# Kernel optimization log

Measured on AMD Instinct MI355X. Metric: run time of the kernel, lower is better.

The kernel has to match this reference:

```python
import jax, jax.numpy as jnp
import numpy as np

G = 8            # group_order
KS = 3           # kernel size
C1, O1 = 1, 16   # gconv1 channels
C2, O2 = 16, 32  # gconv2 channels
HW = 28
NUM_CLASSES = 10


def _bilinear_sample(img, px, py):
    # img: (O, I, K, K); px, py: (K, K) pixel coords; zero padding outside
    # (matches torch grid_sample bilinear, align_corners=False, padding_mode='zeros')
    K = img.shape[-1]
    x0 = jnp.floor(px); y0 = jnp.floor(py)
    wx = px - x0; wy = py - y0
    x0i = x0.astype(jnp.int32); y0i = y0.astype(jnp.int32)

    def gather(yi, xi):
        valid = (yi >= 0) & (yi < K) & (xi >= 0) & (xi < K)
        yc = jnp.clip(yi, 0, K - 1)
        xc = jnp.clip(xi, 0, K - 1)
        return img[:, :, yc, xc] * valid.astype(img.dtype)  # (O,I,K,K)

    return (gather(y0i, x0i) * (1 - wx) * (1 - wy)
            + gather(y0i, x0i + 1) * wx * (1 - wy)
            + gather(y0i + 1, x0i) * (1 - wx) * wy
            + gather(y0i + 1, x0i + 1) * wx * wy)


def _rotated_kernels(base, group_order):
    # Replicates F.affine_grid + F.grid_sample (align_corners=False) for each rotation k.
    K = base.shape[-1]
    coords = (2.0 * jnp.arange(K, dtype=base.dtype) + 1.0) / K - 1.0  # normalized centers
    xs, ys = jnp.meshgrid(coords, coords, indexing='xy')  # x along width, y along height

    def rot_k(k):
        theta = 2.0 * np.pi * k / group_order
        c, s = jnp.cos(theta), jnp.sin(theta)
        gx = c * xs - s * ys   # theta row [cos, -sin, 0]
        gy = s * xs + c * ys   # theta row [sin,  cos, 0]
        px = ((gx + 1.0) * K - 1.0) / 2.0  # unnormalize, align_corners=False
        py = ((gy + 1.0) * K - 1.0) / 2.0
        return _bilinear_sample(base, px, py)

    return jax.vmap(rot_k)(jnp.arange(group_order, dtype=base.dtype))  # (G,O,I,K,K)


def _conv2d(x, w, pad):
    return jax.lax.conv_general_dilated(
        x, w, window_strides=(1, 1), padding=[(pad, pad), (pad, pad)],
        dimension_numbers=('NCHW', 'OIHW', 'NCHW'))


def setup_inputs() -> dict:
    key = jax.random.key(0)
    k1, k2, k3, k4, k5 = jax.random.split(key, 5)
    x = jax.random.normal(k1, (512, C1, HW, HW), dtype=jnp.float32)
    base_weight = jax.random.normal(k2, (O1, C1, KS, KS), dtype=jnp.float32)
    w2 = jax.random.normal(k3, (O2, C2, G, KS, KS), dtype=jnp.float32) * 0.05
    fc_w = jax.random.normal(k4, (NUM_CLASSES, O2 * HW * HW), dtype=jnp.float32) * 0.01
    fc_b = jax.random.normal(k5, (NUM_CLASSES,), dtype=jnp.float32) * 0.01
    return {"x": x, "base_weight": base_weight, "w2": w2, "fc_w": fc_w, "fc_b": fc_b}


def reference(x, base_weight, w2, fc_w, fc_b):
    B = x.shape[0]
    # --- GroupConv2D: steerable rotated kernels, concat along out-channels (k-major) ---
    rk = _rotated_kernels(base_weight, G)           # (G, O1, C1, K, K)
    w1 = rk.reshape(G * O1, C1, KS, KS)
    h = _conv2d(x, w1, 1)                           # (B, G*O1, 28, 28)
    h = jax.nn.relu(h)                              # GroupReLU == plain ReLU

    # --- GroupToGroupConv: circulant structure fused into one conv ---
    # torch: out channel = g*O2 + o (cat dim=1), in channel = c*G + h_idx (view layout)
    g = jnp.arange(G)[:, None]
    hh = jnp.arange(G)[None, :]
    idx = (g - hh) % G                               # (G, G)
    Wc = w2[:, :, idx]                               # (O2, C2, G_g, G_h, K, K)
    Wbig = jnp.transpose(Wc, (2, 0, 1, 3, 4, 5)).reshape(G * O2, C2 * G, KS, KS)
    h2 = _conv2d(h, Wbig, 1)                         # (B, G*O2, 28, 28)
    h2 = jax.nn.relu(h2)

    # --- GroupPooling (mean over the *inner* factor of 8, as in the torch view) ---
    p = h2.reshape(B, (G * O2) // G, G, HW, HW).mean(axis=2)  # (B, 32, 28, 28)

    # --- fc ---
    flat = p.reshape(B, -1)
    return flat @ fc_w.T + fc_b
```

## Files before the change

### kernel.cpp

```cpp
#include <hip/hip_runtime.h>
#include <hip/hip_bf16.h>
#include <cstdint>

#define AS1 __attribute__((address_space(1)))
#define AS3 __attribute__((address_space(3)))

typedef __bf16 bf16x8 __attribute__((ext_vector_type(8)));
typedef float  f32x16 __attribute__((ext_vector_type(16)));

__device__ __forceinline__ void gld_lds16(const void* g, void* l) {
    __builtin_amdgcn_global_load_lds((const AS1 void*)g, (AS3 void*)l, 16, 0, 0);
}

__global__ void k_rot(const float* __restrict__ base, float* __restrict__ w1) {
    int m = threadIdx.x;
    int g = m >> 4, o = m & 15;
    float th = 6.28318530717958647692f * (float)g / 8.0f;
    float c = cosf(th), s = sinf(th);
    for (int i = 0; i < 3; ++i) {
        float ys = (2.0f * i + 1.0f) / 3.0f - 1.0f;
        for (int j = 0; j < 3; ++j) {
            float xs = (2.0f * j + 1.0f) / 3.0f - 1.0f;
            float gx = c * xs - s * ys;
            float gy = s * xs + c * ys;
            float px = ((gx + 1.0f) * 3.0f - 1.0f) * 0.5f;
            float py = ((gy + 1.0f) * 3.0f - 1.0f) * 0.5f;
            float x0 = floorf(px), y0 = floorf(py);
            float wx = px - x0, wy = py - y0;
            int x0i = (int)x0, y0i = (int)y0;
            auto gat = [&](int yi, int xi) -> float {
                bool v = (yi >= 0) && (yi < 3) && (xi >= 0) && (xi < 3);
                int yc = min(max(yi, 0), 2), xc = min(max(xi, 0), 2);
                return v ? base[o * 9 + yc * 3 + xc] : 0.0f;
            };
            w1[m * 9 + i * 3 + j] =
                  gat(y0i, x0i)         * (1.0f - wx) * (1.0f - wy)
                + gat(y0i, x0i + 1)     * wx          * (1.0f - wy)
                + gat(y0i + 1, x0i)     * (1.0f - wx) * wy
                + gat(y0i + 1, x0i + 1) * wx          * wy;
        }
    }
}

__global__ __launch_bounds__(256) void k_conv1(const float* __restrict__ x,
                                               const float* __restrict__ w1g,
                                               const float* __restrict__ w2,
                                               __hip_bfloat16* __restrict__ hl,
                                               __hip_bfloat16* __restrict__ A) {
    int tid = threadIdx.x;

    if (blockIdx.x < 1152) {
        int i = blockIdx.x * 256 + tid;
        int r = i / 1152, k = i - r * 1152;
        int g = r >> 5, o2 = r & 31;
        int kk = k >> 7, cch = k & 127;
        int ky = kk / 3, kx = kk - ky * 3;
        int c2 = cch >> 3, hh = cch & 7;
        int gi = (g - hh) & 7;
        float val = w2[((o2 * 16 + c2) * 8 + gi) * 9 + ky * 3 + kx];
        int half = cch >> 6, kt = cch & 63;
        int t = kk * 2 + half, ks2 = kt >> 4, hi2 = (kt >> 3) & 1, e = kt & 7;
        int mh = r >> 7, i2 = (r >> 5) & 3, row = r & 31;
        int aidx = ((((t * 2 + mh) * 16) + i2 * 4 + ks2) << 9) + ((hi2 << 5) + row) * 8 + e;
        A[aidx] = __float2bfloat16(val);
    }

    __shared__ float w1s[1152];
    for (int i = tid; i < 1152; i += 256) w1s[i] = w1g[i];
    __syncthreads();

    const int c0 = (tid & 15) * 8;
    float wreg[8][9];
#pragma unroll
    for (int cc = 0; cc < 8; ++cc)
#pragma unroll
        for (int k = 0; k < 9; ++k) wreg[cc][k] = w1s[(c0 + cc) * 9 + k];

    const int slot = tid >> 4;
    const int band = blockIdx.x % 15;
    const int b    = blockIdx.x / 15;
    const int yy   = band * 2 + (slot >> 3);
    const int xx0  = (slot & 7) * 4;

    const float* xb = x + b * 784;
    float xv[3][6];
#pragma unroll
    for (int t = 0; t < 3; ++t) {
        int sy = yy - 2 + t;
        bool syok = (sy >= 0) && (sy < 28);
#pragma unroll
        for (int u = 0; u < 6; ++u) {
            int sx = xx0 - 2 + u;
            bool ok = syok && (sx >= 0) && (sx < 28);
            xv[t][u] = ok ? xb[sy * 28 + sx] : 0.0f;
        }
    }

    float acc[4][8];
#pragma unroll
    for (int j = 0; j < 4; ++j)
#pragma unroll
        for (int cc = 0; cc < 8; ++cc) acc[j][cc] = 0.0f;

#pragma unroll
    for (int t = 0; t < 3; ++t)
#pragma unroll
        for (int u = 0; u < 3; ++u) {
#pragma unroll
            for (int j = 0; j < 4; ++j) {
                float xvv = xv[t][j + u];
#pragma unroll
                for (int cc = 0; cc < 8; ++cc)
                    acc[j][cc] += xvv * wreg[cc][t * 3 + u];
            }
        }

#pragma unroll
    for (int j = 0; j < 4; ++j) {
        int xx = xx0 + j;
        if (xx < 30) {
            bool interior = (yy >= 1) && (yy <= 28) && (xx >= 1) && (xx <= 28);
            union { __hip_bfloat16 h[8]; float4 f4; } u;
#pragma unroll
            for (int cc = 0; cc < 8; ++cc)
                u.h[cc] = __float2bfloat16(interior ? fmaxf(acc[j][cc], 0.0f) : 0.0f);
            int pi = b * 900 + yy * 30 + xx;
            *(float4*)(hl + (size_t)pi * 128 + c0) = u.f4;
        }
    }
}

__global__ __launch_bounds__(512, 2) void k_conv2(const __hip_bfloat16* __restrict__ A,
                                                  const __hip_bfloat16* __restrict__ hl,
                                                  __hip_bfloat16* __restrict__ p) {
    __shared__ __align__(16) char smem[131072];

    const int tid  = threadIdx.x;
    const int lane = tid & 63;
    const int w    = tid >> 6;
    const int hi   = lane >> 5;
    const int wqr  = w >> 2;
    const int wqc  = w & 3;

    const int bid = blockIdx.x;
    const int nt  = (bid & 7) * 196 + (bid >> 3);
    const int n0  = nt << 8;

    uint32_t bSrc[2][2], ldsCh[2];
#pragma unroll
    for (int q = 0; q < 2; ++q) {
        int ch = 2 * w + q;
        int rl = ch * 8 + (lane >> 3);
        int ca = (lane & 7) ^ (rl & 7) ^ (ch & 3);
        ldsCh[q] = (uint32_t)(ch * 1024);
#pragma unroll
        for (int hn = 0; hn < 2; ++hn) {
            int n = n0 + hn * 128 + rl;
            int b = n / 784; int rr = n - b * 784;
            int y = rr / 28; int xx = rr - y * 28;
            bSrc[q][hn] = (uint32_t)(((b * 30 + y) * 30 + xx) * 256 + ca * 16);
        }
    }

    uint32_t bRd[2]; int bSw[2];
#pragma unroll
    for (int j = 0; j < 2; ++j) {
        int r = wqc * 64 + j * 32 + (lane & 31);
        bRd[j] = (uint32_t)((r >> 7) * 16384 + (r & 127) * 128);
        bSw[j] = (r & 7) ^ ((r >> 3) & 3);
    }

    const uint32_t aRd = (uint32_t)(wqr * 16384 + lane * 16);

    f32x16 acc[4][2];
#pragma unroll
    for (int i = 0; i < 4; ++i)
#pragma unroll
        for (int j = 0; j < 2; ++j) acc[i][j] = (f32x16)(0.0f);

    const char* Ab = (const char*)A;
    const char* Hb = (const char*)hl;

    auto stage = [&](int tt, char* dst) {
#pragma unroll
        for (int q = 0; q < 4; ++q)
            gld_lds16(Ab + (size_t)tt * 32768 + q * 8192 + tid * 16,
                      dst + q * 8192 + tid * 16);
        int kk = tt >> 1, half = tt & 1;
        int ky = kk / 3, kx = kk - ky * 3;
        uint32_t boff = (uint32_t)((ky * 30 + kx) * 256 + half * 128);
        gld_lds16(Hb + bSrc[0][0] + boff, dst + 32768 + ldsCh[0]);
        gld_lds16(Hb + bSrc[1][0] + boff, dst + 32768 + ldsCh[1]);
        gld_lds16(Hb + bSrc[0][1] + boff, dst + 49152 + ldsCh[0]);
        gld_lds16(Hb + bSrc[1][1] + boff, dst + 49152 + ldsCh[1]);
    };

    stage(0, smem);

#pragma unroll 1
    for (int t = 0; t < 17; ++t) {
        __syncthreads();
        char* cur = smem + ((t & 1) << 16);
        const char* LA = cur + aRd;
        const char* LB = cur + 32768;
        stage(t + 1, smem + (((t + 1) & 1) << 16));

        bf16x8 aF[4][4], bF[4][2];
#pragma unroll
        for (int ksp = 0; ksp < 2; ++ksp) {
#pragma unroll
            for (int i = 0; i < 4; ++i)
                aF[ksp][i] = *(const bf16x8*)(LA + ((i * 4 + ksp) << 10));
#pragma unroll
            for (int j = 0; j < 2; ++j)
                bF[ksp][j] = *(const bf16x8*)(LB + bRd[j] + ((uint32_t)((ksp * 2 + hi) ^ bSw[j]) << 4));
        }

#pragma unroll
        for (int ks = 0; ks < 4; ++ks) {
            if (ks < 2) {
#pragma unroll
                for (int i = 0; i < 4; ++i)
                    aF[ks + 2][i] = *(const bf16x8*)(LA + ((i * 4 + ks + 2) << 10));
#pragma unroll
                for (int j = 0; j < 2; ++j)
                    bF[ks + 2][j] = *(const bf16x8*)(LB + bRd[j] + ((uint32_t)(((ks + 2) * 2 + hi) ^ bSw[j]) << 4));
            }
#pragma unroll
            for (int i = 0; i < 4; ++i)
#pragma unroll
                for (int j = 0; j < 2; ++j)
                    acc[i][j] = __builtin_amdgcn_mfma_f32_32x32x16_bf16(aF[ks][i], bF[ks][j], acc[i][j], 0, 0, 0);
        }

#pragma unroll
        for (int r = 0; r < 4; ++r) {
            __builtin_amdgcn_sched_group_barrier(0x030, 4, 0);
            __builtin_amdgcn_sched_group_barrier(0x100, 3, 0);
        }
#pragma unroll
        for (int r = 0; r < 6; ++r) {
            __builtin_amdgcn_sched_group_barrier(0x008, 1, 0);
            __builtin_amdgcn_sched_group_barrier(0x100, 1, 0);
        }
        __builtin_amdgcn_sched_group_barrier(0x008, 2, 0);
#pragma unroll
        for (int r = 0; r < 6; ++r) {
            __builtin_amdgcn_sched_group_barrier(0x008, 1, 0);
            __builtin_amdgcn_sched_group_barrier(0x100, 1, 0);
        }
        __builtin_amdgcn_sched_group_barrier(0x008, 2, 0);
        __builtin_amdgcn_sched_group_barrier(0x008, 16, 0);
    }

    {
        __syncthreads();
        char* cur = smem + 65536;
        const char* LA = cur + aRd;
        const char* LB = cur + 32768;

        bf16x8 aF[4][4], bF[4][2];
#pragma unroll
        for (int ksp = 0; ksp < 2; ++ksp) {
#pragma unroll
            for (int i = 0; i < 4; ++i)
                aF[ksp][i] = *(const bf16x8*)(LA + ((i * 4 + ksp) << 10));
#pragma unroll
            for (int j = 0; j < 2; ++j)
                bF[ksp][j] = *(const bf16x8*)(LB + bRd[j] + ((uint32_t)((ksp * 2 + hi) ^ bSw[j]) << 4));
        }
#pragma unroll
        for (int ks = 0; ks < 4; ++ks) {
            if (ks < 2) {
#pragma unroll
                for (int i = 0; i < 4; ++i)
                    aF[ks + 2][i] = *(const bf16x8*)(LA + ((i * 4 + ks + 2) << 10));
#pragma unroll
                for (int j = 0; j < 2; ++j)
                    bF[ks + 2][j] = *(const bf16x8*)(LB + bRd[j] + ((uint32_t)(((ks + 2) * 2 + hi) ^ bSw[j]) << 4));
            }
#pragma unroll
            for (int i = 0; i < 4; ++i)
#pragma unroll
                for (int j = 0; j < 2; ++j)
                    acc[i][j] = __builtin_amdgcn_mfma_f32_32x32x16_bf16(aF[ks][i], bF[ks][j], acc[i][j], 0, 0, 0);
        }
    }

#pragma unroll
    for (int i = 0; i < 4; ++i) {
#pragma unroll
        for (int j = 0; j < 2; ++j) {
            f32x16 v = acc[i][j];
#pragma unroll
            for (int u = 0; u < 4; ++u) {
                float sv = fmaxf(v[4*u], 0.0f) + fmaxf(v[4*u+1], 0.0f)
                         + fmaxf(v[4*u+2], 0.0f) + fmaxf(v[4*u+3], 0.0f);
                sv += __shfl_xor(sv, 32, 64);
                if (hi == 0) {
                    int a = wqr * 16 + i * 4 + u;
                    int n = n0 + wqc * 64 + j * 32 + (lane & 31);
                    int b = n / 784; int rr = n - b * 784;
                    p[(b * 32 + a) * 784 + rr] = __float2bfloat16(sv * 0.125f);
                }
            }
        }
    }
}

__global__ __launch_bounds__(256) void k_fc(const __hip_bfloat16* __restrict__ p,
                                            const float* __restrict__ fw,
                                            const float* __restrict__ fb,
                                            float* __restrict__ out) {
    int b = blockIdx.x >> 2, ks = blockIdx.x & 3;
    int tid = threadIdx.x;
    const bf16x8* pb = (const bf16x8*)(p + (size_t)b * 25088);
    const float4* w4 = (const float4*)fw;
    float acc[10] = {};
    for (int t = ks * 784 + tid; t < (ks + 1) * 784; t += 256) {
        union { bf16x8 v; __hip_bfloat16 h[8]; } u;
        u.v = pb[t];
        float vf[8];
#pragma unroll
        for (int e = 0; e < 8; ++e) vf[e] = __bfloat162float(u.h[e]);
#pragma unroll
        for (int c = 0; c < 10; ++c) {
            float4 u0 = w4[c * 6272 + 2 * t];
            float4 u1 = w4[c * 6272 + 2 * t + 1];
            acc[c] += vf[0] * u0.x + vf[1] * u0.y + vf[2] * u0.z + vf[3] * u0.w
                    + vf[4] * u1.x + vf[5] * u1.y + vf[6] * u1.z + vf[7] * u1.w;
        }
    }
    __shared__ float red[10][4];
    int lane = tid & 63, wv = tid >> 6;
#pragma unroll
    for (int c = 0; c < 10; ++c) {
        float s = acc[c];
#pragma unroll
        for (int o = 32; o > 0; o >>= 1) s += __shfl_down(s, o, 64);
        if (lane == 0) red[c][wv] = s;
    }
    __syncthreads();
    if (tid < 10) {
        float s = red[tid][0] + red[tid][1] + red[tid][2] + red[tid][3];
        if (ks == 0) s += fb[tid];
        atomicAdd(&out[b * 10 + tid], s);
    }
}

extern "C" void kernel_launch(void* const* d_in, const int* in_sizes, int n_in,
                              void* d_out, int out_size, void* d_ws, size_t ws_size,
                              hipStream_t stream) {
    const float* x  = (const float*)d_in[0];
    const float* bw = (const float*)d_in[1];
    const float* w2 = (const float*)d_in[2];
    const float* fw = (const float*)d_in[3];
    const float* fb = (const float*)d_in[4];
    float* out = (float*)d_out;
    char* ws = (char*)d_ws;

    float*          w1   = (float*)(ws);
    __hip_bfloat16* Amat = (__hip_bfloat16*)(ws + 4608);
    __hip_bfloat16* hl   = (__hip_bfloat16*)(ws + 594432);
    __hip_bfloat16* p    = (__hip_bfloat16*)(ws + 118563328);

    hipMemsetAsync(d_out, 0, (size_t)out_size * sizeof(float), stream);
    k_rot  <<<1,    128, 0, stream>>>(bw, w1);
    k_conv1<<<7680, 256, 0, stream>>>(x, w1, w2, hl, Amat);
    k_conv2<<<1568, 512, 0, stream>>>(Amat, hl, p);
    k_fc   <<<2048, 256, 0, stream>>>(p, fw, fb, out);
}
```

Baseline: 365.7 us.

## Load conv2 weight fragments directly from global, halve LDS footprint

The conv2 kernel no longer stages the weight matrix A through shared memory. Each wave now reads its A fragments straight from global memory (L1/L2 cached, since every block shares the same weights), and these loads are software-pipelined a step ahead across iterations. Shared memory holds only the double-buffered activation tile, which halves LDS use per block and cuts LDS write and read traffic. The cost is higher global-load latency on the MFMA critical path, plus a hand-tuned scheduling barrier pattern to interleave the VMEM loads with the MFMAs.

```diff
diff --git a/kernel.cpp b/kernel.cpp
--- a/kernel.cpp
+++ b/kernel.cpp
@@ -133,7 +133,7 @@
 __global__ __launch_bounds__(512, 2) void k_conv2(const __hip_bfloat16* __restrict__ A,
                                                   const __hip_bfloat16* __restrict__ hl,
                                                   __hip_bfloat16* __restrict__ p) {
-    __shared__ __align__(16) char smem[131072];
+    __shared__ __align__(16) char smem[65536];
 
     const int tid  = threadIdx.x;
     const int lane = tid & 63;
@@ -170,7 +170,8 @@
         bSw[j] = (r & 7) ^ ((r >> 3) & 3);
     }
 
-    const uint32_t aRd = (uint32_t)(wqr * 16384 + lane * 16);
+    const char* Ab = (const char*)A;
+    const char* gA = Ab + wqr * 16384 + lane * 16;
 
     f32x16 acc[4][2];
 #pragma unroll
@@ -178,113 +179,145 @@
 #pragma unroll
         for (int j = 0; j < 2; ++j) acc[i][j] = (f32x16)(0.0f);
 
-    const char* Ab = (const char*)A;
     const char* Hb = (const char*)hl;
 
-    auto stage = [&](int tt, char* dst) {
-#pragma unroll
-        for (int q = 0; q < 4; ++q)
-            gld_lds16(Ab + (size_t)tt * 32768 + q * 8192 + tid * 16,
-                      dst + q * 8192 + tid * 16);
+    auto stageB = [&](int tt, char* dst) {
         int kk = tt >> 1, half = tt & 1;
         int ky = kk / 3, kx = kk - ky * 3;
         uint32_t boff = (uint32_t)((ky * 30 + kx) * 256 + half * 128);
-        gld_lds16(Hb + bSrc[0][0] + boff, dst + 32768 + ldsCh[0]);
-        gld_lds16(Hb + bSrc[1][0] + boff, dst + 32768 + ldsCh[1]);
-        gld_lds16(Hb + bSrc[0][1] + boff, dst + 49152 + ldsCh[0]);
-        gld_lds16(Hb + bSrc[1][1] + boff, dst + 49152 + ldsCh[1]);
+        gld_lds16(Hb + bSrc[0][0] + boff, dst + ldsCh[0]);
+        gld_lds16(Hb + bSrc[1][0] + boff, dst + ldsCh[1]);
+        gld_lds16(Hb + bSrc[0][1] + boff, dst + 16384 + ldsCh[0]);
+        gld_lds16(Hb + bSrc[1][1] + boff, dst + 16384 + ldsCh[1]);
     };
 
-    stage(0, smem);
+    stageB(0, smem);
+    bf16x8 aF[4][4], bF[4][2];
+#pragma unroll
+    for (int ksp = 0; ksp < 2; ++ksp)
+#pragma unroll
+        for (int i = 0; i < 4; ++i)
+            aF[ksp][i] = *(const bf16x8*)(gA + ((i * 4 + ksp) << 10));
 
 #pragma unroll 1
     for (int t = 0; t < 17; ++t) {
         __syncthreads();
-        char* cur = smem + ((t & 1) << 16);
-        const char* LA = cur + aRd;
-        const char* LB = cur + 32768;
-        stage(t + 1, smem + (((t + 1) & 1) << 16));
-
-        bf16x8 aF[4][4], bF[4][2];
-#pragma unroll
-        for (int ksp = 0; ksp < 2; ++ksp) {
+        const char* LB = smem + ((t & 1) << 15);
+        stageB(t + 1, smem + (((t + 1) & 1) << 15));
+        const char* gAt = gA + (size_t)t * 32768;
+
+#pragma unroll
+        for (int ksp = 0; ksp < 2; ++ksp)
+#pragma unroll
+            for (int j = 0; j < 2; ++j)
+                bF[ksp][j] = *(const bf16x8*)(LB + bRd[j] + ((uint32_t)((ksp * 2 + hi) ^ bSw[j]) << 4));
+
+#pragma unroll
+        for (int i = 0; i < 4; ++i)
+            aF[2][i] = *(const bf16x8*)(gAt + ((i * 4 + 2) << 10));
+#pragma unroll
+        for (int j = 0; j < 2; ++j)
+            bF[2][j] = *(const bf16x8*)(LB + bRd[j] + ((uint32_t)((4 + hi) ^ bSw[j]) << 4));
+#pragma unroll
+        for (int i = 0; i < 4; ++i)
+#pragma unroll
+            for (int j = 0; j < 2; ++j)
+                acc[i][j] = __builtin_amdgcn_mfma_f32_32x32x16_bf16(aF[0][i], bF[0][j], acc[i][j], 0, 0, 0);
+
+#pragma unroll
+        for (int i = 0; i < 4; ++i)
+            aF[3][i] = *(const bf16x8*)(gAt + ((i * 4 + 3) << 10));
+#pragma unroll
+        for (int j = 0; j < 2; ++j)
+            bF[3][j] = *(const bf16x8*)(LB + bRd[j] + ((uint32_t)((6 + hi) ^ bSw[j]) << 4));
+#pragma unroll
+        for (int i = 0; i < 4; ++i)
+#pragma unroll
+            for (int j = 0; j < 2; ++j)
+                acc[i][j] = __builtin_amdgcn_mfma_f32_32x32x16_bf16(aF[1][i], bF[1][j], acc[i][j], 0, 0, 0);
+
+#pragma unroll
+        for (int i = 0; i < 4; ++i)
+            aF[0][i] = *(const bf16x8*)(gAt + 32768 + ((i * 4 + 0) << 10));
+#pragma unroll
+        for (int i = 0; i < 4; ++i)
+#pragma unroll
+            for (int j = 0; j < 2; ++j)
+                acc[i][j] = __builtin_amdgcn_mfma_f32_32x32x16_bf16(aF[2][i], bF[2][j], acc[i][j], 0, 0, 0);
+
+#pragma unroll
+        for (int i = 0; i < 4; ++i)
+            aF[1][i] = *(const bf16x8*)(gAt + 32768 + ((i * 4 + 1) << 10));
+#pragma unroll
+        for (int i = 0; i < 4; ++i)
+#pragma unroll
+            for (int j = 0; j < 2; ++j)
+                acc[i][j] = __builtin_amdgcn_mfma_f32_32x32x16_bf16(aF[3][i], bF[3][j], acc[i][j], 0, 0, 0);
+
+        __builtin_amdgcn_sched_group_barrier(0x030, 4, 0);
+        __builtin_amdgcn_sched_group_barrier(0x100, 4, 0);
+#pragma unroll
+        for (int r = 0; r < 4; ++r) {
+            __builtin_amdgcn_sched_group_barrier(0x008, 1, 0);
+            __builtin_amdgcn_sched_group_barrier(0x030, 1, 0);
+        }
+#pragma unroll
+        for (int r = 0; r < 2; ++r) {
+            __builtin_amdgcn_sched_group_barrier(0x008, 1, 0);
+            __builtin_amdgcn_sched_group_barrier(0x100, 1, 0);
+        }
+        __builtin_amdgcn_sched_group_barrier(0x008, 2, 0);
+#pragma unroll
+        for (int r = 0; r < 4; ++r) {
+            __builtin_amdgcn_sched_group_barrier(0x008, 1, 0);
+            __builtin_amdgcn_sched_group_barrier(0x030, 1, 0);
+        }
+#pragma unroll
+        for (int r = 0; r < 2; ++r) {
+            __builtin_amdgcn_sched_group_barrier(0x008, 1, 0);
+            __builtin_amdgcn_sched_group_barrier(0x100, 1, 0);
+        }
+        __builtin_amdgcn_sched_group_barrier(0x008, 2, 0);
+#pragma unroll
+        for (int r = 0; r < 4; ++r) {
+            __builtin_amdgcn_sched_group_barrier(0x008, 1, 0);
+            __builtin_amdgcn_sched_group_barrier(0x030, 1, 0);
+        }
+        __builtin_amdgcn_sched_group_barrier(0x008, 4, 0);
+#pragma unroll
+        for (int r = 0; r < 4; ++r) {
+            __builtin_amdgcn_sched_group_barrier(0x008, 1, 0);
+            __builtin_amdgcn_sched_group_barrier(0x030, 1, 0);
+        }
+        __builtin_amdgcn_sched_group_barrier(0x008, 4, 0);
+    }
+
+    {
+        __syncthreads();
+        const char* LB = smem + 32768;
+        const char* gAt = gA + (size_t)17 * 32768;
+
+#pragma unroll
+        for (int ksp = 0; ksp < 2; ++ksp)
+#pragma unroll
+            for (int j = 0; j < 2; ++j)
+                bF[ksp][j] = *(const bf16x8*)(LB + bRd[j] + ((uint32_t)((ksp * 2 + hi) ^ bSw[j]) << 4));
+#pragma unroll
+        for (int ksp = 2; ksp < 4; ++ksp) {
 #pragma unroll
             for (int i = 0; i < 4; ++i)
-                aF[ksp][i] = *(const bf16x8*)(LA + ((i * 4 + ksp) << 10));
+                aF[ksp][i] = *(const bf16x8*)(gAt + ((i * 4 + ksp) << 10));
 #pragma unroll
             for (int j = 0; j < 2; ++j)
                 bF[ksp][j] = *(const bf16x8*)(LB + bRd[j] + ((uint32_t)((ksp * 2 + hi) ^ bSw[j]) << 4));
         }
-
-#pragma unroll
-        for (int ks = 0; ks < 4; ++ks) {
-            if (ks < 2) {
-#pragma unroll
-                for (int i = 0; i < 4; ++i)
-                    aF[ks + 2][i] = *(const bf16x8*)(LA + ((i * 4 + ks + 2) << 10));
-#pragma unroll
-                for (int j = 0; j < 2; ++j)
-                    bF[ks + 2][j] = *(const bf16x8*)(LB + bRd[j] + ((uint32_t)(((ks + 2) * 2 + hi) ^ bSw[j]) << 4));
-            }
+#pragma unroll
+        for (int ks = 0; ks < 4; ++ks)
 #pragma unroll
             for (int i = 0; i < 4; ++i)
 #pragma unroll
                 for (int j = 0; j < 2; ++j)
                     acc[i][j] = __builtin_amdgcn_mfma_f32_32x32x16_bf16(aF[ks][i], bF[ks][j], acc[i][j], 0, 0, 0);
-        }
-
-#pragma unroll
-        for (int r = 0; r < 4; ++r) {
-            __builtin_amdgcn_sched_group_barrier(0x030, 4, 0);
-            __builtin_amdgcn_sched_group_barrier(0x100, 3, 0);
-        }
-#pragma unroll
-        for (int r = 0; r < 6; ++r) {
-            __builtin_amdgcn_sched_group_barrier(0x008, 1, 0);
-            __builtin_amdgcn_sched_group_barrier(0x100, 1, 0);
-        }
-        __builtin_amdgcn_sched_group_barrier(0x008, 2, 0);
-#pragma unroll
-        for (int r = 0; r < 6; ++r) {
-            __builtin_amdgcn_sched_group_barrier(0x008, 1, 0);
-            __builtin_amdgcn_sched_group_barrier(0x100, 1, 0);
-        }
-        __builtin_amdgcn_sched_group_barrier(0x008, 2, 0);
-        __builtin_amdgcn_sched_group_barrier(0x008, 16, 0);
-    }
-
-    {
-        __syncthreads();
-        char* cur = smem + 65536;
-        const char* LA = cur + aRd;
-        const char* LB = cur + 32768;
-
-        bf16x8 aF[4][4], bF[4][2];
-#pragma unroll
-        for (int ksp = 0; ksp < 2; ++ksp) {
-#pragma unroll
-            for (int i = 0; i < 4; ++i)
-                aF[ksp][i] = *(const bf16x8*)(LA + ((i * 4 + ksp) << 10));
-#pragma unroll
-            for (int j = 0; j < 2; ++j)
-                bF[ksp][j] = *(const bf16x8*)(LB + bRd[j] + ((uint32_t)((ksp * 2 + hi) ^ bSw[j]) << 4));
-        }
-#pragma unroll
-        for (int ks = 0; ks < 4; ++ks) {
-            if (ks < 2) {
-#pragma unroll
-                for (int i = 0; i < 4; ++i)
-                    aF[ks + 2][i] = *(const bf16x8*)(LA + ((i * 4 + ks + 2) << 10));
-#pragma unroll
-                for (int j = 0; j < 2; ++j)
-                    bF[ks + 2][j] = *(const bf16x8*)(LB + bRd[j] + ((uint32_t)(((ks + 2) * 2 + hi) ^ bSw[j]) << 4));
-            }
-#pragma unroll
-            for (int i = 0; i < 4; ++i)
-#pragma unroll
-                for (int j = 0; j < 2; ++j)
-                    acc[i][j] = __builtin_amdgcn_mfma_f32_32x32x16_bf16(aF[ks][i], bF[ks][j], acc[i][j], 0, 0, 0);
-        }
     }
 
 #pragma unroll
```

Result: no change. 362.5 us (-0.9%).
